# Kernel tuning notes

Hardware: AMD Instinct MI355X
Metric: run time of the kernel (lower is better)

Reference implementation:

```python
import jax, jax.numpy as jnp
import numpy as np

N = 20000      # total nodes (miRNA_number); first 504 are circRNAs
FM = 128       # feature dim (args.fm)
H = 8          # attention heads
OC = 128       # conv out_channels
E = 160000     # random edges (self loops added inside reference)
NEG_SLOPE = 0.2
CIRC = 504


def setup_inputs() -> dict:
    key = jax.random.key(0)
    ks = jax.random.split(key, 12)
    s_in = 1.0 / np.sqrt(FM)
    return {
        'x': jax.random.normal(ks[0], (N, FM), jnp.float32),
        'edge_index': jax.random.randint(ks[1], (2, E), 0, N, jnp.int64),
        'W1': jax.random.normal(ks[2], (FM, H * FM), jnp.float32) * s_in,
        'as1': jax.random.normal(ks[3], (H, FM), jnp.float32) * 0.1,
        'ad1': jax.random.normal(ks[4], (H, FM), jnp.float32) * 0.1,
        'b1': jnp.zeros((FM,), jnp.float32),
        'W2': jax.random.normal(ks[5], (FM, H * FM), jnp.float32) * s_in,
        'as2': jax.random.normal(ks[6], (H, FM), jnp.float32) * 0.1,
        'ad2': jax.random.normal(ks[7], (H, FM), jnp.float32) * 0.1,
        'b2': jnp.zeros((FM,), jnp.float32),
        'Wc': jax.random.normal(ks[8], (OC, 2, FM), jnp.float32) * s_in,
        'bc': jnp.zeros((OC,), jnp.float32),
    }


def gat_conv(x, src, dst, W, a_src, a_dst, b):
    # PyG GATConv, heads=H, concat=False (head mean), add_self_loops done by caller
    h = (x @ W).reshape(N, H, FM)                       # [N,H,F]
    s = jnp.einsum('nhf,hf->nh', h, a_src)              # alpha_src per node
    d = jnp.einsum('nhf,hf->nh', h, a_dst)              # alpha_dst per node
    e = jax.nn.leaky_relu(s[src] + d[dst], NEG_SLOPE)   # [E,H]
    m = jax.ops.segment_max(e, dst, num_segments=N)     # segment softmax (stable)
    ee = jnp.exp(e - m[dst])
    den = jax.ops.segment_sum(ee, dst, num_segments=N)
    alpha = ee / (den[dst] + 1e-16)                     # [E,H]
    out = jax.ops.segment_sum(h[src] * alpha[:, :, None], dst, num_segments=N)
    return out.mean(axis=1) + b                         # [N,F]


def reference(x, edge_index, W1, as1, ad1, b1, W2, as2, ad2, b2, Wc, bc):
    loops = jnp.arange(N, dtype=edge_index.dtype)
    src = jnp.concatenate([edge_index[0], loops])
    dst = jnp.concatenate([edge_index[1], loops])
    x1 = jax.nn.relu(gat_conv(x, src, dst, W1, as1, ad1, b1))
    x2 = jax.nn.relu(gat_conv(x1, src, dst, W2, as2, ad2, b2))
    # cat((x1,x2),dim=1).t().view(1, 2, FM, N) -> channels = [x1.T, x2.T]
    XM = jnp.stack([x1.T, x2.T], axis=0)                # [2,FM,N]
    feat = jnp.einsum('ckn,ock->on', XM, Wc) + bc[:, None]  # Conv1d kernel (FM,1)
    emb = feat.T                                        # [N,OC]
    circ, mir = emb[:CIRC], emb[CIRC:]
    return circ @ mir.T, circ, mir
```

## Files before the change

### kernel.cpp

```cpp
#include <hip/hip_runtime.h>
#include <math.h>

constexpr int NN   = 20000;
constexpr int FM   = 128;
constexpr int NH   = 8;
constexpr int HF   = NH * FM;
constexpr int EE   = 160000;
constexpr int ET   = EE + NN;
constexpr int OC   = 128;
constexpr int CIRC = 504;
constexpr int MIRN = NN - CIRC;
constexpr float NEG = 0.2f;

constexpr size_t OFF_CIRC = (size_t)CIRC * MIRN;
constexpr size_t OFF_MIR  = OFF_CIRC + (size_t)CIRC * OC;

__device__ __forceinline__ float rl_f(float v, int lane) {
  return __uint_as_float(__builtin_amdgcn_readlane(__float_as_uint(v), lane));
}
__device__ __forceinline__ int rl_i(int v, int lane) {
  return __builtin_amdgcn_readlane(v, lane);
}
__device__ __forceinline__ unsigned short bf16_rne(float x) {
  unsigned u = __float_as_uint(x);
  return (unsigned short)((u + 0x7FFFu + ((u >> 16) & 1u)) >> 16);
}
__device__ __forceinline__ float blo(unsigned u) { return __uint_as_float(u << 16); }
__device__ __forceinline__ float bhi(unsigned u) { return __uint_as_float(u & 0xFFFF0000u); }

__global__ void k_init_counts(int* __restrict__ cnt) {
  int i = blockIdx.x * blockDim.x + threadIdx.x;
  if (i < NN) cnt[i] = 1;
}

__global__ void k_count(const int* __restrict__ ei, int* __restrict__ cnt) {
  int e = blockIdx.x * blockDim.x + threadIdx.x;
  if (e < EE) atomicAdd(&cnt[ei[EE + e]], 1);
}

__global__ __launch_bounds__(1024) void k_scan(const int* __restrict__ cnt,
                                               int* __restrict__ rs,
                                               int* __restrict__ cur) {
  __shared__ int part[1024];
  const int t = threadIdx.x;
  const int SEG = (NN + 1023) / 1024;
  int lo = t * SEG, hi = min(NN, lo + SEG);
  int s = 0;
  for (int i = lo; i < hi; ++i) s += cnt[i];
  part[t] = s;
  __syncthreads();
  for (int off = 1; off < 1024; off <<= 1) {
    int v = 0;
    if (t >= off) v = part[t - off];
    __syncthreads();
    part[t] += v;
    __syncthreads();
  }
  int run = (t == 0) ? 0 : part[t - 1];
  for (int i = lo; i < hi; ++i) {
    int c = cnt[i];
    rs[i] = run;
    cur[i] = run;
    run += c;
  }
  if (t == 1023) rs[NN] = part[1023];
}

__global__ void k_fill(const int* __restrict__ ei, int* __restrict__ cur,
                       int* __restrict__ csrc) {
  int i = blockIdx.x * blockDim.x + threadIdx.x;
  if (i >= ET) return;
  int s, d;
  if (i < EE) { s = ei[i]; d = ei[EE + i]; }
  else        { s = i - EE; d = s; }
  int p = atomicAdd(&cur[d], 1);
  csrc[p] = s;
}

__global__ __launch_bounds__(256) void k_gemm_xw(const float* __restrict__ X,
                                                 const float* __restrict__ W,
                                                 const float* __restrict__ Asc,
                                                 const float* __restrict__ Adc,
                                                 unsigned short* __restrict__ H16,
                                                 float* __restrict__ Sv,
                                                 float* __restrict__ Dv,
                                                 int M) {
  __shared__ float xs[64][129];
  const int t = threadIdx.x;
  const int row0 = blockIdx.x * 64;
  const int col0 = blockIdx.y * 256;
#pragma unroll
  for (int it = 0; it < 8; ++it) {
    int f4 = it * 256 + t;
    int r = f4 >> 5;
    int c = (f4 & 31) << 2;
    float4 v = make_float4(0.f, 0.f, 0.f, 0.f);
    int gr = row0 + r;
    if (gr < M) v = *reinterpret_cast<const float4*>(X + (size_t)gr * FM + c);
    xs[r][c] = v.x; xs[r][c + 1] = v.y; xs[r][c + 2] = v.z; xs[r][c + 3] = v.w;
  }
  __syncthreads();
  const int tr = (t >> 5) << 3;
  const int tc = (t & 31) << 3;
  float acc[8][8];
#pragma unroll
  for (int r = 0; r < 8; ++r)
#pragma unroll
    for (int c = 0; c < 8; ++c) acc[r][c] = 0.f;
  const float* Wp = W + col0 + tc;
  for (int kk = 0; kk < FM; ++kk) {
    float4 b0 = *reinterpret_cast<const float4*>(Wp + (size_t)kk * HF);
    float4 b1 = *reinterpret_cast<const float4*>(Wp + (size_t)kk * HF + 4);
    float bv[8] = {b0.x, b0.y, b0.z, b0.w, b1.x, b1.y, b1.z, b1.w};
    float av[8];
#pragma unroll
    for (int r = 0; r < 8; ++r) av[r] = xs[tr + r][kk];
#pragma unroll
    for (int r = 0; r < 8; ++r)
#pragma unroll
      for (int c = 0; c < 8; ++c) acc[r][c] += av[r] * bv[c];
  }
#pragma unroll
  for (int r = 0; r < 8; ++r) {
    int gr = row0 + tr + r;
    if (gr < M) {
      union { unsigned short us[8]; uint4 v; } pk;
#pragma unroll
      for (int c = 0; c < 8; ++c) pk.us[c] = bf16_rne(acc[r][c]);
      *reinterpret_cast<uint4*>(H16 + (size_t)gr * HF + col0 + tc) = pk.v;
    }
  }
  const int hd = 2 * blockIdx.y + ((t & 31) >> 4);
  const int fc = (t & 15) << 3;
  float asv[8], adv[8];
#pragma unroll
  for (int c = 0; c < 8; ++c) {
    asv[c] = Asc[hd * FM + fc + c];
    adv[c] = Adc[hd * FM + fc + c];
  }
#pragma unroll
  for (int r = 0; r < 8; ++r) {
    float s = 0.f, d = 0.f;
#pragma unroll
    for (int c = 0; c < 8; ++c) {
      s += acc[r][c] * asv[c];
      d += acc[r][c] * adv[c];
    }
#pragma unroll
    for (int mo = 1; mo <= 8; mo <<= 1) {
      s += __shfl_xor(s, mo, 64);
      d += __shfl_xor(d, mo, 64);
    }
    int gr = row0 + tr + r;
    if ((t & 15) == 0 && gr < M) {
      Sv[gr * 8 + hd] = s;
      Dv[gr * 8 + hd] = d;
    }
  }
}

__global__ __launch_bounds__(256) void k_agg(const unsigned short* __restrict__ H16,
                                             const float* __restrict__ Sv,
                                             const float* __restrict__ Dv,
                                             const int* __restrict__ rs,
                                             const int* __restrict__ csrc,
                                             const float* __restrict__ bias,
                                             float* __restrict__ Xo) {
  const int wave = threadIdx.x >> 6;
  const int lane = threadIdx.x & 63;
  const int n = blockIdx.x * 4 + wave;
  if (n >= NN) return;
  const int r0 = rs[n];
  const int deg = rs[n + 1] - r0;
  const int j = lane >> 3, h = lane & 7;
  const int h0 = lane >> 4;
  const int boff = h0 * FM + (lane & 15) * 8;
  const float dvh = Dv[n * 8 + h];

  float m = -INFINITY, l = 0.f;
  float4 acc[4];
#pragma unroll
  for (int q = 0; q < 4; ++q) acc[q] = make_float4(0.f, 0.f, 0.f, 0.f);

  for (int base = 0; base < deg; base += 8) {
    const int cnt = deg - base;
    int sj = csrc[r0 + min(base + j, deg - 1)];
    float lg = (j < cnt) ? (Sv[sj * 8 + h] + dvh) : -INFINITY;
    lg = lg > 0.f ? lg : NEG * lg;
    float cm = lg;
    cm = fmaxf(cm, __shfl_xor(cm, 8, 64));
    cm = fmaxf(cm, __shfl_xor(cm, 16, 64));
    cm = fmaxf(cm, __shfl_xor(cm, 32, 64));
    float mn = fmaxf(m, cm);
    float fs = expf(m - mn);
    float p = expf(lg - mn);
    float cs = p;
    cs += __shfl_xor(cs, 8, 64);
    cs += __shfl_xor(cs, 16, 64);
    cs += __shfl_xor(cs, 32, 64);
    l = l * fs + cs;
    m = mn;
    float f0 = __shfl(fs, h0, 64);
    float f1 = __shfl(fs, h0 + 4, 64);
    acc[0].x *= f0; acc[0].y *= f0; acc[0].z *= f0; acc[0].w *= f0;
    acc[1].x *= f0; acc[1].y *= f0; acc[1].z *= f0; acc[1].w *= f0;
    acc[2].x *= f1; acc[2].y *= f1; acc[2].z *= f1; acc[2].w *= f1;
    acc[3].x *= f1; acc[3].y *= f1; acc[3].z *= f1; acc[3].w *= f1;
#pragma unroll
    for (int jj = 0; jj < 8; ++jj) {
      if (jj < cnt) {
        int se = rl_i(sj, jj * 8);
        const uint4* hp = reinterpret_cast<const uint4*>(H16 + (size_t)se * HF + boff);
        uint4 v0 = hp[0];
        uint4 v1 = hp[64];
        float pe0 = __shfl(p, jj * 8 + h0, 64);
        float pe1 = __shfl(p, jj * 8 + h0 + 4, 64);
        acc[0].x += pe0 * blo(v0.x); acc[0].y += pe0 * bhi(v0.x);
        acc[0].z += pe0 * blo(v0.y); acc[0].w += pe0 * bhi(v0.y);
        acc[1].x += pe0 * blo(v0.z); acc[1].y += pe0 * bhi(v0.z);
        acc[1].z += pe0 * blo(v0.w); acc[1].w += pe0 * bhi(v0.w);
        acc[2].x += pe1 * blo(v1.x); acc[2].y += pe1 * bhi(v1.x);
        acc[2].z += pe1 * blo(v1.y); acc[2].w += pe1 * bhi(v1.y);
        acc[3].x += pe1 * blo(v1.z); acc[3].y += pe1 * bhi(v1.z);
        acc[3].z += pe1 * blo(v1.w); acc[3].w += pe1 * bhi(v1.w);
      }
    }
  }
  float inv0 = 1.0f / (__shfl(l, h0, 64) + 1e-16f);
  float inv1 = 1.0f / (__shfl(l, h0 + 4, 64) + 1e-16f);
  float o[8];
  o[0] = acc[0].x * inv0 + acc[2].x * inv1;
  o[1] = acc[0].y * inv0 + acc[2].y * inv1;
  o[2] = acc[0].z * inv0 + acc[2].z * inv1;
  o[3] = acc[0].w * inv0 + acc[2].w * inv1;
  o[4] = acc[1].x * inv0 + acc[3].x * inv1;
  o[5] = acc[1].y * inv0 + acc[3].y * inv1;
  o[6] = acc[1].z * inv0 + acc[3].z * inv1;
  o[7] = acc[1].w * inv0 + acc[3].w * inv1;
#pragma unroll
  for (int k = 0; k < 8; ++k) {
    o[k] += __shfl_xor(o[k], 16, 64);
    o[k] += __shfl_xor(o[k], 32, 64);
  }
  if (lane < 16) {
    const int f0i = lane * 8;
    float4 b0 = *reinterpret_cast<const float4*>(bias + f0i);
    float4 b1 = *reinterpret_cast<const float4*>(bias + f0i + 4);
    float4 w0, w1;
    w0.x = fmaxf(o[0] * 0.125f + b0.x, 0.f);
    w0.y = fmaxf(o[1] * 0.125f + b0.y, 0.f);
    w0.z = fmaxf(o[2] * 0.125f + b0.z, 0.f);
    w0.w = fmaxf(o[3] * 0.125f + b0.w, 0.f);
    w1.x = fmaxf(o[4] * 0.125f + b1.x, 0.f);
    w1.y = fmaxf(o[5] * 0.125f + b1.y, 0.f);
    w1.z = fmaxf(o[6] * 0.125f + b1.z, 0.f);
    w1.w = fmaxf(o[7] * 0.125f + b1.w, 0.f);
    *reinterpret_cast<float4*>(Xo + (size_t)n * FM + f0i) = w0;
    *reinterpret_cast<float4*>(Xo + (size_t)n * FM + f0i + 4) = w1;
  }
}

__global__ void k_transpose_wc(const float* __restrict__ Wc, float* __restrict__ WcT) {
  int i = blockIdx.x * blockDim.x + threadIdx.x;
  if (i < OC * 2 * FM) {
    int o = i / (2 * FM), k = i % (2 * FM);
    WcT[k * OC + o] = Wc[i];
  }
}

__global__ __launch_bounds__(256) void k_emb(const float* __restrict__ X1,
                                             const float* __restrict__ X2,
                                             const float* __restrict__ WcT,
                                             const float* __restrict__ bc,
                                             float* __restrict__ Out) {
  __shared__ float xs[64][129];
  const int t = threadIdx.x;
  const int row0 = blockIdx.x * 64;
  const int tr = (t >> 5) << 3;
  const int tc = (t & 31) << 2;
  float acc[8][4] = {};
  for (int half = 0; half < 2; ++half) {
    const float* Xs = half ? X2 : X1;
    __syncthreads();
#pragma unroll
    for (int it = 0; it < 8; ++it) {
      int f4 = it * 256 + t;
      int r = f4 >> 5;
      int c = (f4 & 31) << 2;
      int gr = row0 + r;
      float4 v = make_float4(0.f, 0.f, 0.f, 0.f);
      if (gr < NN) v = *reinterpret_cast<const float4*>(Xs + (size_t)gr * FM + c);
      xs[r][c] = v.x; xs[r][c + 1] = v.y; xs[r][c + 2] = v.z; xs[r][c + 3] = v.w;
    }
    __syncthreads();
    const float* Wp = WcT + (size_t)half * FM * OC;
    for (int kk = 0; kk < FM; ++kk) {
      float4 b = *reinterpret_cast<const float4*>(Wp + kk * OC + tc);
      float av[8];
#pragma unroll
      for (int r = 0; r < 8; ++r) av[r] = xs[tr + r][kk];
#pragma unroll
      for (int r = 0; r < 8; ++r) {
        acc[r][0] += av[r] * b.x;
        acc[r][1] += av[r] * b.y;
        acc[r][2] += av[r] * b.z;
        acc[r][3] += av[r] * b.w;
      }
    }
  }
  float4 bcv = *reinterpret_cast<const float4*>(bc + tc);
#pragma unroll
  for (int r = 0; r < 8; ++r) {
    int gr = row0 + tr + r;
    if (gr < NN) {
      float4 o;
      o.x = acc[r][0] + bcv.x;
      o.y = acc[r][1] + bcv.y;
      o.z = acc[r][2] + bcv.z;
      o.w = acc[r][3] + bcv.w;
      float* dst = (gr < CIRC)
                       ? (Out + OFF_CIRC + (size_t)gr * OC + tc)
                       : (Out + OFF_MIR + (size_t)(gr - CIRC) * OC + tc);
      *reinterpret_cast<float4*>(dst) = o;
    }
  }
}

__global__ __launch_bounds__(256) void k_outer(const float* __restrict__ A,
                                               const float* __restrict__ B,
                                               float* __restrict__ C) {
  __shared__ float As[64][65];
  __shared__ float Bs[64][65];
  const int t = threadIdx.x;
  const int i0 = blockIdx.y * 64;
  const int j0 = blockIdx.x * 64;
  const int tx = t & 15, ty = t >> 4;
  float acc[4][4] = {};
  for (int kh = 0; kh < 2; ++kh) {
    __syncthreads();
#pragma unroll
    for (int it = 0; it < 4; ++it) {
      int f4 = it * 256 + t;
      int r = f4 >> 4;
      int c = (f4 & 15) << 2;
      float4 v = make_float4(0.f, 0.f, 0.f, 0.f);
      if (i0 + r < CIRC)
        v = *reinterpret_cast<const float4*>(A + (size_t)(i0 + r) * OC + kh * 64 + c);
      As[r][c] = v.x; As[r][c + 1] = v.y; As[r][c + 2] = v.z; As[r][c + 3] = v.w;
      float4 w = make_float4(0.f, 0.f, 0.f, 0.f);
      if (j0 + r < MIRN)
        w = *reinterpret_cast<const float4*>(B + (size_t)(j0 + r) * OC + kh * 64 + c);
      Bs[r][c] = w.x; Bs[r][c + 1] = w.y; Bs[r][c + 2] = w.z; Bs[r][c + 3] = w.w;
    }
    __syncthreads();
    for (int kk = 0; kk < 64; ++kk) {
      float a[4], b[4];
#pragma unroll
      for (int r = 0; r < 4; ++r) a[r] = As[ty * 4 + r][kk];
#pragma unroll
      for (int c = 0; c < 4; ++c) b[c] = Bs[tx * 4 + c][kk];
#pragma unroll
      for (int r = 0; r < 4; ++r)
#pragma unroll
        for (int c = 0; c < 4; ++c) acc[r][c] += a[r] * b[c];
    }
  }
#pragma unroll
  for (int r = 0; r < 4; ++r) {
    int i = i0 + ty * 4 + r;
    if (i >= CIRC) break;
#pragma unroll
    for (int c = 0; c < 4; ++c) {
      int j = j0 + tx * 4 + c;
      if (j < MIRN) C[(size_t)i * MIRN + j] = acc[r][c];
    }
  }
}

static inline size_t alignup(size_t v) { return (v + 255) & ~(size_t)255; }

extern "C" void kernel_launch(void* const* d_in, const int* in_sizes, int n_in,
                              void* d_out, int out_size, void* d_ws, size_t ws_size,
                              hipStream_t stream) {
  const float* x   = (const float*)d_in[0];
  const int*   ei  = (const int*)d_in[1];
  const float* W1  = (const float*)d_in[2];
  const float* as1 = (const float*)d_in[3];
  const float* ad1 = (const float*)d_in[4];
  const float* b1  = (const float*)d_in[5];
  const float* W2  = (const float*)d_in[6];
  const float* as2 = (const float*)d_in[7];
  const float* ad2 = (const float*)d_in[8];
  const float* b2  = (const float*)d_in[9];
  const float* Wc  = (const float*)d_in[10];
  const float* bc  = (const float*)d_in[11];
  float* out = (float*)d_out;

  char* w = (char*)d_ws;
  size_t off = 0;
  unsigned short* H16 = (unsigned short*)(w + off); off = alignup(off + (size_t)NN * HF * 2);
  float* Sbuf = (float*)(w + off); off = alignup(off + (size_t)NN * NH * 4);
  float* Dbuf = (float*)(w + off); off = alignup(off + (size_t)NN * NH * 4);
  float* X1   = (float*)(w + off); off = alignup(off + (size_t)NN * FM * 4);
  float* X2   = (float*)(w + off); off = alignup(off + (size_t)NN * FM * 4);
  float* WcT  = (float*)(w + off); off = alignup(off + (size_t)OC * 2 * FM * 4);
  int* counts = (int*)(w + off);   off = alignup(off + (size_t)NN * 4);
  int* rowst  = (int*)(w + off);   off = alignup(off + (size_t)(NN + 1) * 4);
  int* cursor = (int*)(w + off);   off = alignup(off + (size_t)NN * 4);
  int* csrsrc = (int*)(w + off);   off = alignup(off + (size_t)ET * 4);

  k_init_counts<<<(NN + 255) / 256, 256, 0, stream>>>(counts);
  k_count<<<(EE + 255) / 256, 256, 0, stream>>>(ei, counts);
  k_scan<<<1, 1024, 0, stream>>>(counts, rowst, cursor);
  k_fill<<<(ET + 255) / 256, 256, 0, stream>>>(ei, cursor, csrsrc);

  dim3 gGemm((NN + 63) / 64, HF / 256);
  k_gemm_xw<<<gGemm, 256, 0, stream>>>(x, W1, as1, ad1, H16, Sbuf, Dbuf, NN);
  k_agg<<<(NN + 3) / 4, 256, 0, stream>>>(H16, Sbuf, Dbuf, rowst, csrsrc, b1, X1);
  k_gemm_xw<<<gGemm, 256, 0, stream>>>(X1, W2, as2, ad2, H16, Sbuf, Dbuf, NN);
  k_agg<<<(NN + 3) / 4, 256, 0, stream>>>(H16, Sbuf, Dbuf, rowst, csrsrc, b2, X2);
  k_transpose_wc<<<(OC * 2 * FM + 255) / 256, 256, 0, stream>>>(Wc, WcT);
  k_emb<<<(NN + 63) / 64, 256, 0, stream>>>(X1, X2, WcT, bc, out);
  k_outer<<<dim3((MIRN + 63) / 64, (CIRC + 63) / 64), 256, 0, stream>>>(
      out + OFF_CIRC, out + OFF_MIR, out);
}
```

Measured before the change: 492.1 us.

## Replace FP32 SIMT projection GEMM with split-bf16 MFMA GEMM

Replaces the scalar FP32 X·W GEMM with an MFMA bf16 kernel that emulates FP32 accuracy with a hi/lo split (three MFMAs per K step). Weights are split and transposed once per layer, and the input features are split in a separate kernel. The aggregation kernel now also writes the hi/lo bf16 copy of its output, so the second layer's GEMM gets its operand without an extra pass. This adds prep kernels and workspace, and H16 stores are now scalar 2-byte writes scattered per lane, which may cost memory efficiency.

```diff
diff --git a/kernel.cpp b/kernel.cpp
--- a/kernel.cpp
+++ b/kernel.cpp
@@ -15,9 +15,9 @@
 constexpr size_t OFF_CIRC = (size_t)CIRC * MIRN;
 constexpr size_t OFF_MIR  = OFF_CIRC + (size_t)CIRC * OC;
 
-__device__ __forceinline__ float rl_f(float v, int lane) {
-  return __uint_as_float(__builtin_amdgcn_readlane(__float_as_uint(v), lane));
-}
+typedef __attribute__((ext_vector_type(8))) short bf16x8;
+typedef __attribute__((ext_vector_type(4))) float f32x4;
+
 __device__ __forceinline__ int rl_i(int v, int lane) {
   return __builtin_amdgcn_readlane(v, lane);
 }
@@ -77,86 +77,91 @@
   csrc[p] = s;
 }
 
-__global__ __launch_bounds__(256) void k_gemm_xw(const float* __restrict__ X,
-                                                 const float* __restrict__ W,
-                                                 const float* __restrict__ Asc,
-                                                 const float* __restrict__ Adc,
-                                                 unsigned short* __restrict__ H16,
-                                                 float* __restrict__ Sv,
-                                                 float* __restrict__ Dv,
-                                                 int M) {
-  __shared__ float xs[64][129];
-  const int t = threadIdx.x;
-  const int row0 = blockIdx.x * 64;
-  const int col0 = blockIdx.y * 256;
-#pragma unroll
-  for (int it = 0; it < 8; ++it) {
-    int f4 = it * 256 + t;
-    int r = f4 >> 5;
-    int c = (f4 & 31) << 2;
-    float4 v = make_float4(0.f, 0.f, 0.f, 0.f);
-    int gr = row0 + r;
-    if (gr < M) v = *reinterpret_cast<const float4*>(X + (size_t)gr * FM + c);
-    xs[r][c] = v.x; xs[r][c + 1] = v.y; xs[r][c + 2] = v.z; xs[r][c + 3] = v.w;
-  }
-  __syncthreads();
-  const int tr = (t >> 5) << 3;
-  const int tc = (t & 31) << 3;
-  float acc[8][8];
-#pragma unroll
-  for (int r = 0; r < 8; ++r)
-#pragma unroll
-    for (int c = 0; c < 8; ++c) acc[r][c] = 0.f;
-  const float* Wp = W + col0 + tc;
-  for (int kk = 0; kk < FM; ++kk) {
-    float4 b0 = *reinterpret_cast<const float4*>(Wp + (size_t)kk * HF);
-    float4 b1 = *reinterpret_cast<const float4*>(Wp + (size_t)kk * HF + 4);
-    float bv[8] = {b0.x, b0.y, b0.z, b0.w, b1.x, b1.y, b1.z, b1.w};
-    float av[8];
-#pragma unroll
-    for (int r = 0; r < 8; ++r) av[r] = xs[tr + r][kk];
-#pragma unroll
-    for (int r = 0; r < 8; ++r)
-#pragma unroll
-      for (int c = 0; c < 8; ++c) acc[r][c] += av[r] * bv[c];
-  }
-#pragma unroll
-  for (int r = 0; r < 8; ++r) {
-    int gr = row0 + tr + r;
-    if (gr < M) {
-      union { unsigned short us[8]; uint4 v; } pk;
-#pragma unroll
-      for (int c = 0; c < 8; ++c) pk.us[c] = bf16_rne(acc[r][c]);
-      *reinterpret_cast<uint4*>(H16 + (size_t)gr * HF + col0 + tc) = pk.v;
-    }
-  }
-  const int hd = 2 * blockIdx.y + ((t & 31) >> 4);
-  const int fc = (t & 15) << 3;
-  float asv[8], adv[8];
-#pragma unroll
-  for (int c = 0; c < 8; ++c) {
-    asv[c] = Asc[hd * FM + fc + c];
-    adv[c] = Adc[hd * FM + fc + c];
-  }
-#pragma unroll
-  for (int r = 0; r < 8; ++r) {
-    float s = 0.f, d = 0.f;
-#pragma unroll
-    for (int c = 0; c < 8; ++c) {
-      s += acc[r][c] * asv[c];
-      d += acc[r][c] * adv[c];
-    }
-#pragma unroll
-    for (int mo = 1; mo <= 8; mo <<= 1) {
-      s += __shfl_xor(s, mo, 64);
-      d += __shfl_xor(d, mo, 64);
-    }
-    int gr = row0 + tr + r;
-    if ((t & 15) == 0 && gr < M) {
-      Sv[gr * 8 + hd] = s;
-      Dv[gr * 8 + hd] = d;
-    }
-  }
+__global__ void k_prep_w(const float* __restrict__ W,
+                         unsigned short* __restrict__ WThi,
+                         unsigned short* __restrict__ WTlo) {
+  int i = blockIdx.x * blockDim.x + threadIdx.x;
+  if (i >= FM * HF) return;
+  int k = i >> 10, n = i & 1023;
+  float v = W[i];
+  unsigned short h = bf16_rne(v);
+  WThi[(size_t)n * FM + k] = h;
+  WTlo[(size_t)n * FM + k] = bf16_rne(v - blo(h));
+}
+
+__global__ void k_split_x(const float* __restrict__ X,
+                          unsigned short* __restrict__ Xhi,
+                          unsigned short* __restrict__ Xlo) {
+  int i = blockIdx.x * blockDim.x + threadIdx.x;
+  if (i >= NN * FM) return;
+  float v = X[i];
+  unsigned short h = bf16_rne(v);
+  Xhi[i] = h;
+  Xlo[i] = bf16_rne(v - blo(h));
+}
+
+__global__ __launch_bounds__(256) void k_gemm_mfma(
+    const unsigned short* __restrict__ Xhi, const unsigned short* __restrict__ Xlo,
+    const unsigned short* __restrict__ WThi, const unsigned short* __restrict__ WTlo,
+    const float* __restrict__ Asc, const float* __restrict__ Adc,
+    unsigned short* __restrict__ H16, float* __restrict__ Sv,
+    float* __restrict__ Dv) {
+  const int lane = threadIdx.x & 63;
+  const int wq   = threadIdx.x >> 6;
+  const int m0   = blockIdx.x * 16;
+  const int ri   = lane & 15;
+  const int kg   = lane >> 4;
+
+  bf16x8 Ah[4], Al[4];
+  const unsigned short* xb = Xhi + (size_t)(m0 + ri) * FM + kg * 8;
+  const unsigned short* xl = Xlo + (size_t)(m0 + ri) * FM + kg * 8;
+#pragma unroll
+  for (int ks = 0; ks < 4; ++ks) {
+    Ah[ks] = *reinterpret_cast<const bf16x8*>(xb + ks * 32);
+    Al[ks] = *reinterpret_cast<const bf16x8*>(xl + ks * 32);
+  }
+  float sacc[2][4] = {}, dacc[2][4] = {};
+  for (int ct = 0; ct < 16; ++ct) {
+    const int gc = wq * 256 + ct * 16 + ri;
+    const unsigned short* wb = WThi + (size_t)gc * FM + kg * 8;
+    const unsigned short* wl = WTlo + (size_t)gc * FM + kg * 8;
+    f32x4 a0 = {0.f, 0.f, 0.f, 0.f}, a1 = a0, a2 = a0;
+#pragma unroll
+    for (int ks = 0; ks < 4; ++ks) {
+      bf16x8 Bh = *reinterpret_cast<const bf16x8*>(wb + ks * 32);
+      bf16x8 Bl = *reinterpret_cast<const bf16x8*>(wl + ks * 32);
+      a0 = __builtin_amdgcn_mfma_f32_16x16x32_bf16(Ah[ks], Bh, a0, 0, 0, 0);
+      a1 = __builtin_amdgcn_mfma_f32_16x16x32_bf16(Al[ks], Bh, a1, 0, 0, 0);
+      a2 = __builtin_amdgcn_mfma_f32_16x16x32_bf16(Ah[ks], Bl, a2, 0, 0, 0);
+    }
+    const int hh = ct >> 3;
+    const float as_ = Asc[(wq * 2 + hh) * FM + (gc & 127)];
+    const float ad_ = Adc[(wq * 2 + hh) * FM + (gc & 127)];
+#pragma unroll
+    for (int r = 0; r < 4; ++r) {
+      float v = a0[r] + a1[r] + a2[r];
+      int m = m0 + kg * 4 + r;
+      H16[(size_t)m * HF + gc] = bf16_rne(v);
+      sacc[hh][r] += v * as_;
+      dacc[hh][r] += v * ad_;
+    }
+  }
+#pragma unroll
+  for (int hh = 0; hh < 2; ++hh)
+#pragma unroll
+    for (int r = 0; r < 4; ++r) {
+      float s = sacc[hh][r], d = dacc[hh][r];
+#pragma unroll
+      for (int mo = 1; mo <= 8; mo <<= 1) {
+        s += __shfl_xor(s, mo, 64);
+        d += __shfl_xor(d, mo, 64);
+      }
+      if (ri == 0) {
+        int m = m0 + kg * 4 + r;
+        Sv[m * NH + wq * 2 + hh] = s;
+        Dv[m * NH + wq * 2 + hh] = d;
+      }
+    }
 }
 
 __global__ __launch_bounds__(256) void k_agg(const unsigned short* __restrict__ H16,
@@ -165,7 +170,9 @@
                                              const int* __restrict__ rs,
                                              const int* __restrict__ csrc,
                                              const float* __restrict__ bias,
-                                             float* __restrict__ Xo) {
+                                             float* __restrict__ Xo,
+                                             unsigned short* __restrict__ XhiO,
+                                             unsigned short* __restrict__ XloO) {
   const int wave = threadIdx.x >> 6;
   const int lane = threadIdx.x & 63;
   const int n = blockIdx.x * 4 + wave;
@@ -244,19 +251,22 @@
   }
   if (lane < 16) {
     const int f0i = lane * 8;
-    float4 b0 = *reinterpret_cast<const float4*>(bias + f0i);
-    float4 b1 = *reinterpret_cast<const float4*>(bias + f0i + 4);
-    float4 w0, w1;
-    w0.x = fmaxf(o[0] * 0.125f + b0.x, 0.f);
-    w0.y = fmaxf(o[1] * 0.125f + b0.y, 0.f);
-    w0.z = fmaxf(o[2] * 0.125f + b0.z, 0.f);
-    w0.w = fmaxf(o[3] * 0.125f + b0.w, 0.f);
-    w1.x = fmaxf(o[4] * 0.125f + b1.x, 0.f);
-    w1.y = fmaxf(o[5] * 0.125f + b1.y, 0.f);
-    w1.z = fmaxf(o[6] * 0.125f + b1.z, 0.f);
-    w1.w = fmaxf(o[7] * 0.125f + b1.w, 0.f);
+    float vals[8];
+    union { unsigned short us[8]; uint4 v; } ph, pl;
+#pragma unroll
+    for (int k = 0; k < 8; ++k) {
+      float bv = bias[f0i + k];
+      vals[k] = fmaxf(o[k] * 0.125f + bv, 0.f);
+      unsigned short hh = bf16_rne(vals[k]);
+      ph.us[k] = hh;
+      pl.us[k] = bf16_rne(vals[k] - blo(hh));
+    }
+    float4 w0 = make_float4(vals[0], vals[1], vals[2], vals[3]);
+    float4 w1 = make_float4(vals[4], vals[5], vals[6], vals[7]);
     *reinterpret_cast<float4*>(Xo + (size_t)n * FM + f0i) = w0;
     *reinterpret_cast<float4*>(Xo + (size_t)n * FM + f0i + 4) = w1;
+    *reinterpret_cast<uint4*>(XhiO + (size_t)n * FM + f0i) = ph.v;
+    *reinterpret_cast<uint4*>(XloO + (size_t)n * FM + f0i) = pl.v;
   }
 }
 
@@ -398,7 +408,11 @@
 
   char* w = (char*)d_ws;
   size_t off = 0;
-  unsigned short* H16 = (unsigned short*)(w + off); off = alignup(off + (size_t)NN * HF * 2);
+  unsigned short* H16  = (unsigned short*)(w + off); off = alignup(off + (size_t)NN * HF * 2);
+  unsigned short* Xhi  = (unsigned short*)(w + off); off = alignup(off + (size_t)NN * FM * 2);
+  unsigned short* Xlo  = (unsigned short*)(w + off); off = alignup(off + (size_t)NN * FM * 2);
+  unsigned short* WThi = (unsigned short*)(w + off); off = alignup(off + (size_t)HF * FM * 2);
+  unsigned short* WTlo = (unsigned short*)(w + off); off = alignup(off + (size_t)HF * FM * 2);
   float* Sbuf = (float*)(w + off); off = alignup(off + (size_t)NN * NH * 4);
   float* Dbuf = (float*)(w + off); off = alignup(off + (size_t)NN * NH * 4);
   float* X1   = (float*)(w + off); off = alignup(off + (size_t)NN * FM * 4);
@@ -414,11 +428,17 @@
   k_scan<<<1, 1024, 0, stream>>>(counts, rowst, cursor);
   k_fill<<<(ET + 255) / 256, 256, 0, stream>>>(ei, cursor, csrsrc);
 
-  dim3 gGemm((NN + 63) / 64, HF / 256);
-  k_gemm_xw<<<gGemm, 256, 0, stream>>>(x, W1, as1, ad1, H16, Sbuf, Dbuf, NN);
-  k_agg<<<(NN + 3) / 4, 256, 0, stream>>>(H16, Sbuf, Dbuf, rowst, csrsrc, b1, X1);
-  k_gemm_xw<<<gGemm, 256, 0, stream>>>(X1, W2, as2, ad2, H16, Sbuf, Dbuf, NN);
-  k_agg<<<(NN + 3) / 4, 256, 0, stream>>>(H16, Sbuf, Dbuf, rowst, csrsrc, b2, X2);
+  k_prep_w<<<(FM * HF + 255) / 256, 256, 0, stream>>>(W1, WThi, WTlo);
+  k_split_x<<<(NN * FM + 255) / 256, 256, 0, stream>>>(x, Xhi, Xlo);
+  k_gemm_mfma<<<NN / 16, 256, 0, stream>>>(Xhi, Xlo, WThi, WTlo, as1, ad1,
+                                           H16, Sbuf, Dbuf);
+  k_agg<<<(NN + 3) / 4, 256, 0, stream>>>(H16, Sbuf, Dbuf, rowst, csrsrc, b1,
+                                          X1, Xhi, Xlo);
+  k_prep_w<<<(FM * HF + 255) / 256, 256, 0, stream>>>(W2, WThi, WTlo);
+  k_gemm_mfma<<<NN / 16, 256, 0, stream>>>(Xhi, Xlo, WThi, WTlo, as2, ad2,
+                                           H16, Sbuf, Dbuf);
+  k_agg<<<(NN + 3) / 4, 256, 0, stream>>>(H16, Sbuf, Dbuf, rowst, csrsrc, b2,
+                                          X2, Xhi, Xlo);
   k_transpose_wc<<<(OC * 2 * FM + 255) / 256, 256, 0, stream>>>(Wc, WcT);
   k_emb<<<(NN + 63) / 64, 256, 0, stream>>>(X1, X2, WcT, bc, out);
   k_outer<<<dim3((MIRN + 63) / 64, (CIRC + 63) / 64), 256, 0, stream>>>(
```

After: 560.7 us. +13.9%, slower.
